# Optimization experiments

Hardware: AMD Instinct MI355X
Metric: run time of the kernel (lower is better)

## Reference

```python
import jax, jax.numpy as jnp
import numpy as np

N_SRC = 50000
N_DST = 10000
E = 1600000
H = 1
F = 128
NEG_SLOPE = 0.2  # GAT default leaky_relu slope


def setup_inputs() -> dict:
    key = jax.random.key(0)
    k1, k2, k3, k4, k5, k6 = jax.random.split(key, 6)
    x_src = jax.random.normal(k1, (N_SRC, H, F), dtype=jnp.float32)
    x_dst = jax.random.normal(k2, (N_DST, H, F), dtype=jnp.float32)
    attn_l = jax.random.normal(k3, (1, H, F), dtype=jnp.float32)
    attn_r = jax.random.normal(k4, (1, H, F), dtype=jnp.float32)
    src_idx = jax.random.randint(k5, (E,), 0, N_SRC, dtype=jnp.int64 if jax.config.jax_enable_x64 else jnp.int32)
    dst_idx = jnp.sort(jax.random.randint(k6, (E,), 0, N_DST, dtype=jnp.int64 if jax.config.jax_enable_x64 else jnp.int32))
    return {"x_src": x_src, "x_dst": x_dst, "attn_l": attn_l, "attn_r": attn_r,
            "src_idx": src_idx, "dst_idx": dst_idx}


def reference(x_src, x_dst, attn_l, attn_r, src_idx, dst_idx):
    n_dst = x_dst.shape[0]
    # per-node attention logits: [N, H]
    el = (x_src * attn_l).sum(axis=-1)
    er = (x_dst * attn_r).sum(axis=-1)
    # per-edge score e = leaky_relu(el[u] + er[v]): [E, H]
    e = jax.nn.leaky_relu(el[src_idx] + er[dst_idx], negative_slope=NEG_SLOPE)
    ex = jnp.exp(e)
    # segment-sum over destination neighborhoods: [N_dst, H]
    sum_ex = jax.ops.segment_sum(ex, dst_idx, num_segments=n_dst)
    attention = ex / sum_ex[dst_idx]  # [E, H]
    # attention-weighted gather of src features, scattered to dst: [N_dst, H, F]
    msg = attention[..., None] * x_src[src_idx]
    out = jax.ops.segment_sum(msg, dst_idx, num_segments=n_dst)
    return out
```

## Files before the change

kernel.cpp:

```cpp
#include <hip/hip_runtime.h>
#include <hip/hip_fp16.h>

#define F 128
#define NEG_SLOPE 0.2f

__global__ __launch_bounds__(256)
void prep_kernel(const float* __restrict__ x_src, const float* __restrict__ attn_l,
                 float* __restrict__ el, __half2* __restrict__ xh, int n_src,
                 const float* __restrict__ x_dst, const float* __restrict__ attn_r,
                 float* __restrict__ er, int n_dst,
                 const int* __restrict__ dst_idx, int* __restrict__ offs, int E,
                 int nlog) {
    if ((int)blockIdx.x < nlog) {
        int row  = blockIdx.x * 4 + (threadIdx.x >> 6);
        int lane = threadIdx.x & 63;
        if (row < n_src) {
            float2 xv = *reinterpret_cast<const float2*>(&x_src[(size_t)row * F + lane * 2]);
            float2 av = *reinterpret_cast<const float2*>(&attn_l[lane * 2]);
            if (xh) xh[(size_t)row * (F / 2) + lane] = __floats2half2_rn(xv.x, xv.y);
            float s = xv.x * av.x + xv.y * av.y;
            #pragma unroll
            for (int o = 32; o > 0; o >>= 1) s += __shfl_xor(s, o, 64);
            if (lane == 0) el[row] = s;
        } else if (row < n_src + n_dst) {
            int r = row - n_src;
            float2 xv = *reinterpret_cast<const float2*>(&x_dst[(size_t)r * F + lane * 2]);
            float2 av = *reinterpret_cast<const float2*>(&attn_r[lane * 2]);
            float s = xv.x * av.x + xv.y * av.y;
            #pragma unroll
            for (int o = 32; o > 0; o >>= 1) s += __shfl_xor(s, o, 64);
            if (lane == 0) er[r] = s;
        }
    } else {
        int e = ((int)blockIdx.x - nlog) * 256 + threadIdx.x;
        if (e >= E) return;
        int d = dst_idx[e];
        int prev = (e == 0) ? -1 : dst_idx[e - 1];
        for (int v = prev + 1; v <= d; ++v) offs[v] = e;
        if (e == E - 1)
            for (int v = d + 1; v <= n_dst; ++v) offs[v] = E;
    }
}

template<bool H>
__global__ __launch_bounds__(256)
void gat_aggregate_kernel(const __half2* __restrict__ xh,
                          const float* __restrict__ x_src,
                          const float* __restrict__ el,
                          const float* __restrict__ er,
                          const int* __restrict__ src_idx,
                          const int* __restrict__ offs,
                          float* __restrict__ out, int n_dst) {
    int v = blockIdx.x * 4 + (threadIdx.x >> 6);
    if (v >= n_dst) return;
    int lane = threadIdx.x & 63;
    int g    = lane >> 4;
    int l16  = lane & 15;

    int start = offs[v];
    int end   = offs[v + 1];
    int count = end - start;
    float erv = er[v];

    const float4* x4h = reinterpret_cast<const float4*>(xh);
    const float4* x4f = reinterpret_cast<const float4*>(x_src);

    float a0[8], a1[8];
    #pragma unroll
    for (int k = 0; k < 8; ++k) { a0[k] = 0.f; a1[k] = 0.f; }
    float d0 = 0.f, d1 = 0.f;

    int full = count & ~7;
    for (int it = 0; it < full; it += 8) {
        int e0 = start + it + g;
        int e1 = e0 + 4;
        int s0 = src_idx[e0];
        int s1 = src_idx[e1];
        float l0 = el[s0] + erv, l1 = el[s1] + erv;
        l0 = l0 > 0.f ? l0 : NEG_SLOPE * l0;
        l1 = l1 > 0.f ? l1 : NEG_SLOPE * l1;
        float w0 = __expf(l0), w1 = __expf(l1);
        d0 += w0; d1 += w1;
        if (H) {
            float4 r0 = x4h[(size_t)s0 * (F / 8) + l16];
            float4 r1 = x4h[(size_t)s1 * (F / 8) + l16];
            const __half2* h0 = reinterpret_cast<const __half2*>(&r0);
            const __half2* h1 = reinterpret_cast<const __half2*>(&r1);
            #pragma unroll
            for (int k = 0; k < 4; ++k) {
                float2 f0 = __half22float2(h0[k]);
                float2 f1 = __half22float2(h1[k]);
                a0[2*k]   += w0 * f0.x;  a0[2*k+1] += w0 * f0.y;
                a1[2*k]   += w1 * f1.x;  a1[2*k+1] += w1 * f1.y;
            }
        } else {
            float4 p0 = x4f[(size_t)s0 * (F / 4) + l16 * 2];
            float4 q0 = x4f[(size_t)s0 * (F / 4) + l16 * 2 + 1];
            float4 p1 = x4f[(size_t)s1 * (F / 4) + l16 * 2];
            float4 q1 = x4f[(size_t)s1 * (F / 4) + l16 * 2 + 1];
            a0[0]+=w0*p0.x; a0[1]+=w0*p0.y; a0[2]+=w0*p0.z; a0[3]+=w0*p0.w;
            a0[4]+=w0*q0.x; a0[5]+=w0*q0.y; a0[6]+=w0*q0.z; a0[7]+=w0*q0.w;
            a1[0]+=w1*p1.x; a1[1]+=w1*p1.y; a1[2]+=w1*p1.z; a1[3]+=w1*p1.w;
            a1[4]+=w1*q1.x; a1[5]+=w1*q1.y; a1[6]+=w1*q1.z; a1[7]+=w1*q1.w;
        }
    }
    for (int e = start + full + g; e < end; e += 4) {
        int s = src_idx[e];
        float l = el[s] + erv;
        l = l > 0.f ? l : NEG_SLOPE * l;
        float w = __expf(l);
        d0 += w;
        if (H) {
            float4 r = x4h[(size_t)s * (F / 8) + l16];
            const __half2* h = reinterpret_cast<const __half2*>(&r);
            #pragma unroll
            for (int k = 0; k < 4; ++k) {
                float2 f = __half22float2(h[k]);
                a0[2*k] += w * f.x;  a0[2*k+1] += w * f.y;
            }
        } else {
            float4 p = x4f[(size_t)s * (F / 4) + l16 * 2];
            float4 q = x4f[(size_t)s * (F / 4) + l16 * 2 + 1];
            a0[0]+=w*p.x; a0[1]+=w*p.y; a0[2]+=w*p.z; a0[3]+=w*p.w;
            a0[4]+=w*q.x; a0[5]+=w*q.y; a0[6]+=w*q.z; a0[7]+=w*q.w;
        }
    }
    #pragma unroll
    for (int k = 0; k < 8; ++k) a0[k] += a1[k];
    d0 += d1;

    #pragma unroll
    for (int k = 0; k < 8; ++k) {
        a0[k] += __shfl_xor(a0[k], 16, 64);
        a0[k] += __shfl_xor(a0[k], 32, 64);
    }
    d0 += __shfl_xor(d0, 16, 64);
    d0 += __shfl_xor(d0, 32, 64);

    if (g == 0) {
        float inv = (count > 0) ? 1.f / d0 : 0.f;
        float4 o0 = make_float4(a0[0]*inv, a0[1]*inv, a0[2]*inv, a0[3]*inv);
        float4 o1 = make_float4(a0[4]*inv, a0[5]*inv, a0[6]*inv, a0[7]*inv);
        float4* dst = reinterpret_cast<float4*>(&out[(size_t)v * F + l16 * 8]);
        dst[0] = o0;
        dst[1] = o1;
    }
}

extern "C" void kernel_launch(void* const* d_in, const int* in_sizes, int n_in,
                              void* d_out, int out_size, void* d_ws, size_t ws_size,
                              hipStream_t stream) {
    const float* x_src   = (const float*)d_in[0];
    const float* x_dst   = (const float*)d_in[1];
    const float* attn_l  = (const float*)d_in[2];
    const float* attn_r  = (const float*)d_in[3];
    const int*   src_idx = (const int*)d_in[4];
    const int*   dst_idx = (const int*)d_in[5];

    int n_src = in_sizes[0] / F;
    int n_dst = in_sizes[1] / F;
    int E     = in_sizes[4];

    float* out  = (float*)d_out;
    float* el   = (float*)d_ws;
    float* er   = el + n_src;
    int*   offs = (int*)(er + n_dst);
    uintptr_t p = (uintptr_t)(offs + n_dst + 1);
    p = (p + 15) & ~(uintptr_t)15;
    __half2* xh = (__half2*)p;

    size_t need = (p - (uintptr_t)d_ws) + (size_t)n_src * F * sizeof(__half);
    bool fp16ok = ws_size >= need;

    int nlog = (n_src + n_dst + 3) / 4;
    int noff = (E + 255) / 256;
    prep_kernel<<<nlog + noff, 256, 0, stream>>>(
        x_src, attn_l, el, fp16ok ? xh : nullptr, n_src,
        x_dst, attn_r, er, n_dst, dst_idx, offs, E, nlog);

    int agg_blocks = (n_dst + 3) / 4;
    if (fp16ok) {
        gat_aggregate_kernel<true><<<agg_blocks, 256, 0, stream>>>(
            xh, x_src, el, er, src_idx, offs, out, n_dst);
    } else {
        gat_aggregate_kernel<false><<<agg_blocks, 256, 0, stream>>>(
            nullptr, x_src, el, er, src_idx, offs, out, n_dst);
    }
}
```

Baseline: 86.93 us.

## Assign one block per destination and bucket edges by source range for locality

Each aggregation block now handles a single destination node with 256 threads instead of one wavefront per node. Edges are processed in chunks: weights are computed once into shared memory, then counting-sorted into 8 source-index buckets so that gathers within a chunk hit nearby rows. Partial sums across the four wavefronts are combined through shared memory. This adds several block barriers, shared atomics and more blocks per launch, in exchange for intended gather locality and higher per-node parallelism. With about 160 edges per node, all of them fit in one chunk.

```diff
diff --git a/kernel.cpp b/kernel.cpp
--- a/kernel.cpp
+++ b/kernel.cpp
@@ -3,6 +3,9 @@
 
 #define F 128
 #define NEG_SLOPE 0.2f
+#define NB 8
+#define CH 512
+#define NGR 16
 
 __global__ __launch_bounds__(256)
 void prep_kernel(const float* __restrict__ x_src, const float* __restrict__ attn_l,
@@ -50,18 +53,26 @@
                           const float* __restrict__ er,
                           const int* __restrict__ src_idx,
                           const int* __restrict__ offs,
-                          float* __restrict__ out, int n_dst) {
-    int v = blockIdx.x * 4 + (threadIdx.x >> 6);
-    if (v >= n_dst) return;
-    int lane = threadIdx.x & 63;
-    int g    = lane >> 4;
-    int l16  = lane & 15;
+                          float* __restrict__ out, int bdiv) {
+    int v   = blockIdx.x;
+    int tid = threadIdx.x;
+    int g   = tid >> 4;
+    int l16 = tid & 15;
 
     int start = offs[v];
     int end   = offs[v + 1];
     int count = end - start;
     float erv = er[v];
 
+    __shared__ int   sidx[CH];
+    __shared__ float sw[CH];
+    __shared__ int   bidx[CH];
+    __shared__ float bw[CH];
+    __shared__ int   cnt[NB];
+    __shared__ int   cur[NB];
+    __shared__ float part[4][F];
+    __shared__ float pden[4];
+
     const float4* x4h = reinterpret_cast<const float4*>(xh);
     const float4* x4f = reinterpret_cast<const float4*>(x_src);
 
@@ -70,61 +81,86 @@
     for (int k = 0; k < 8; ++k) { a0[k] = 0.f; a1[k] = 0.f; }
     float d0 = 0.f, d1 = 0.f;
 
-    int full = count & ~7;
-    for (int it = 0; it < full; it += 8) {
-        int e0 = start + it + g;
-        int e1 = e0 + 4;
-        int s0 = src_idx[e0];
-        int s1 = src_idx[e1];
-        float l0 = el[s0] + erv, l1 = el[s1] + erv;
-        l0 = l0 > 0.f ? l0 : NEG_SLOPE * l0;
-        l1 = l1 > 0.f ? l1 : NEG_SLOPE * l1;
-        float w0 = __expf(l0), w1 = __expf(l1);
-        d0 += w0; d1 += w1;
-        if (H) {
-            float4 r0 = x4h[(size_t)s0 * (F / 8) + l16];
-            float4 r1 = x4h[(size_t)s1 * (F / 8) + l16];
-            const __half2* h0 = reinterpret_cast<const __half2*>(&r0);
-            const __half2* h1 = reinterpret_cast<const __half2*>(&r1);
-            #pragma unroll
-            for (int k = 0; k < 4; ++k) {
-                float2 f0 = __half22float2(h0[k]);
-                float2 f1 = __half22float2(h1[k]);
-                a0[2*k]   += w0 * f0.x;  a0[2*k+1] += w0 * f0.y;
-                a1[2*k]   += w1 * f1.x;  a1[2*k+1] += w1 * f1.y;
+    for (int base = start; base < end; base += CH) {
+        int n = min(CH, end - base);
+        if (tid < NB) cnt[tid] = 0;
+        __syncthreads();
+
+        for (int i = tid; i < n; i += 256) {
+            int s = src_idx[base + i];
+            float l = el[s] + erv;
+            l = l > 0.f ? l : NEG_SLOPE * l;
+            sidx[i] = s;
+            sw[i]   = __expf(l);
+            atomicAdd(&cnt[s / bdiv], 1);
+        }
+        __syncthreads();
+        if (tid < NB) {
+            int acc = 0;
+            for (int b = 0; b < tid; ++b) acc += cnt[b];
+            cur[tid] = acc;
+        }
+        __syncthreads();
+        for (int i = tid; i < n; i += 256) {
+            int s = sidx[i];
+            int slot = atomicAdd(&cur[s / bdiv], 1);
+            bidx[slot] = s;
+            bw[slot]   = sw[i];
+        }
+        __syncthreads();
+
+        int full = n & ~(2 * NGR - 1);
+        for (int it = 0; it < full; it += 2 * NGR) {
+            int s0 = bidx[it + g];
+            int s1 = bidx[it + NGR + g];
+            float w0 = bw[it + g];
+            float w1 = bw[it + NGR + g];
+            d0 += w0; d1 += w1;
+            if (H) {
+                float4 r0 = x4h[(size_t)s0 * (F / 8) + l16];
+                float4 r1 = x4h[(size_t)s1 * (F / 8) + l16];
+                const __half2* h0 = reinterpret_cast<const __half2*>(&r0);
+                const __half2* h1 = reinterpret_cast<const __half2*>(&r1);
+                #pragma unroll
+                for (int k = 0; k < 4; ++k) {
+                    float2 f0 = __half22float2(h0[k]);
+                    float2 f1 = __half22float2(h1[k]);
+                    a0[2*k]   += w0 * f0.x;  a0[2*k+1] += w0 * f0.y;
+                    a1[2*k]   += w1 * f1.x;  a1[2*k+1] += w1 * f1.y;
+                }
+            } else {
+                float4 p0 = x4f[(size_t)s0 * (F/4) + l16*2];
+                float4 q0 = x4f[(size_t)s0 * (F/4) + l16*2 + 1];
+                float4 p1 = x4f[(size_t)s1 * (F/4) + l16*2];
+                float4 q1 = x4f[(size_t)s1 * (F/4) + l16*2 + 1];
+                a0[0]+=w0*p0.x; a0[1]+=w0*p0.y; a0[2]+=w0*p0.z; a0[3]+=w0*p0.w;
+                a0[4]+=w0*q0.x; a0[5]+=w0*q0.y; a0[6]+=w0*q0.z; a0[7]+=w0*q0.w;
+                a1[0]+=w1*p1.x; a1[1]+=w1*p1.y; a1[2]+=w1*p1.z; a1[3]+=w1*p1.w;
+                a1[4]+=w1*q1.x; a1[5]+=w1*q1.y; a1[6]+=w1*q1.z; a1[7]+=w1*q1.w;
             }
-        } else {
-            float4 p0 = x4f[(size_t)s0 * (F / 4) + l16 * 2];
-            float4 q0 = x4f[(size_t)s0 * (F / 4) + l16 * 2 + 1];
-            float4 p1 = x4f[(size_t)s1 * (F / 4) + l16 * 2];
-            float4 q1 = x4f[(size_t)s1 * (F / 4) + l16 * 2 + 1];
-            a0[0]+=w0*p0.x; a0[1]+=w0*p0.y; a0[2]+=w0*p0.z; a0[3]+=w0*p0.w;
-            a0[4]+=w0*q0.x; a0[5]+=w0*q0.y; a0[6]+=w0*q0.z; a0[7]+=w0*q0.w;
-            a1[0]+=w1*p1.x; a1[1]+=w1*p1.y; a1[2]+=w1*p1.z; a1[3]+=w1*p1.w;
-            a1[4]+=w1*q1.x; a1[5]+=w1*q1.y; a1[6]+=w1*q1.z; a1[7]+=w1*q1.w;
-        }
-    }
-    for (int e = start + full + g; e < end; e += 4) {
-        int s = src_idx[e];
-        float l = el[s] + erv;
-        l = l > 0.f ? l : NEG_SLOPE * l;
-        float w = __expf(l);
-        d0 += w;
-        if (H) {
-            float4 r = x4h[(size_t)s * (F / 8) + l16];
-            const __half2* h = reinterpret_cast<const __half2*>(&r);
-            #pragma unroll
-            for (int k = 0; k < 4; ++k) {
-                float2 f = __half22float2(h[k]);
-                a0[2*k] += w * f.x;  a0[2*k+1] += w * f.y;
+        }
+        for (int it = full + g; it < n; it += NGR) {
+            int s  = bidx[it];
+            float w = bw[it];
+            d0 += w;
+            if (H) {
+                float4 r = x4h[(size_t)s * (F / 8) + l16];
+                const __half2* h = reinterpret_cast<const __half2*>(&r);
+                #pragma unroll
+                for (int k = 0; k < 4; ++k) {
+                    float2 f = __half22float2(h[k]);
+                    a0[2*k] += w * f.x;  a0[2*k+1] += w * f.y;
+                }
+            } else {
+                float4 p = x4f[(size_t)s * (F/4) + l16*2];
+                float4 q = x4f[(size_t)s * (F/4) + l16*2 + 1];
+                a0[0]+=w*p.x; a0[1]+=w*p.y; a0[2]+=w*p.z; a0[3]+=w*p.w;
+                a0[4]+=w*q.x; a0[5]+=w*q.y; a0[6]+=w*q.z; a0[7]+=w*q.w;
             }
-        } else {
-            float4 p = x4f[(size_t)s * (F / 4) + l16 * 2];
-            float4 q = x4f[(size_t)s * (F / 4) + l16 * 2 + 1];
-            a0[0]+=w*p.x; a0[1]+=w*p.y; a0[2]+=w*p.z; a0[3]+=w*p.w;
-            a0[4]+=w*q.x; a0[5]+=w*q.y; a0[6]+=w*q.z; a0[7]+=w*q.w;
-        }
-    }
+        }
+        __syncthreads();
+    }
+
     #pragma unroll
     for (int k = 0; k < 8; ++k) a0[k] += a1[k];
     d0 += d1;
@@ -137,13 +173,20 @@
     d0 += __shfl_xor(d0, 16, 64);
     d0 += __shfl_xor(d0, 32, 64);
 
-    if (g == 0) {
-        float inv = (count > 0) ? 1.f / d0 : 0.f;
-        float4 o0 = make_float4(a0[0]*inv, a0[1]*inv, a0[2]*inv, a0[3]*inv);
-        float4 o1 = make_float4(a0[4]*inv, a0[5]*inv, a0[6]*inv, a0[7]*inv);
-        float4* dst = reinterpret_cast<float4*>(&out[(size_t)v * F + l16 * 8]);
-        dst[0] = o0;
-        dst[1] = o1;
+    int wid  = tid >> 6;
+    int lane = tid & 63;
+    if ((lane >> 4) == 0) {
+        #pragma unroll
+        for (int k = 0; k < 8; ++k) part[wid][l16 * 8 + k] = a0[k];
+        if (l16 == 0) pden[wid] = d0;
+    }
+    __syncthreads();
+
+    if (tid < F) {
+        float t = 0.f, dd = 0.f;
+        #pragma unroll
+        for (int w = 0; w < 4; ++w) { t += part[w][tid]; dd += pden[w]; }
+        out[(size_t)v * F + tid] = (count > 0) ? t / dd : 0.f;
     }
 }
 
@@ -178,12 +221,12 @@
         x_src, attn_l, el, fp16ok ? xh : nullptr, n_src,
         x_dst, attn_r, er, n_dst, dst_idx, offs, E, nlog);
 
-    int agg_blocks = (n_dst + 3) / 4;
+    int bdiv = (n_src + NB - 1) / NB;
     if (fp16ok) {
-        gat_aggregate_kernel<true><<<agg_blocks, 256, 0, stream>>>(
-            xh, x_src, el, er, src_idx, offs, out, n_dst);
+        gat_aggregate_kernel<true><<<n_dst, 256, 0, stream>>>(
+            xh, x_src, el, er, src_idx, offs, out, bdiv);
     } else {
-        gat_aggregate_kernel<false><<<agg_blocks, 256, 0, stream>>>(
-            nullptr, x_src, el, er, src_idx, offs, out, n_dst);
+        gat_aggregate_kernel<false><<<n_dst, 256, 0, stream>>>(
+            nullptr, x_src, el, er, src_idx, offs, out, bdiv);
     }
 }
```

Result: faster. 80.09 us (-7.9%).

## Partition edges by source-node range and aggregate in cache-sized passes

Applied to the files above, without the earlier changes.

Adds a reorder kernel that buckets each destination's edges into four source-index ranges, then runs the aggregation in four passes, one per range. Each pass only gathers from about a quarter of the fp16 feature table, so that slice should stay resident in the L2 or last-level cache. In exchange it adds a reorder kernel with many block syncs, extra launches, and re-reads and re-writes of the output and a denominator buffer between passes.

```diff
diff --git a/kernel.cpp b/kernel.cpp
--- a/kernel.cpp
+++ b/kernel.cpp
@@ -3,6 +3,7 @@
 
 #define F 128
 #define NEG_SLOPE 0.2f
+#define NB 4
 
 __global__ __launch_bounds__(256)
 void prep_kernel(const float* __restrict__ x_src, const float* __restrict__ attn_l,
@@ -42,24 +43,72 @@
     }
 }
 
+__global__ __launch_bounds__(256)
+void reorder_kernel(const int* __restrict__ src_idx, const int* __restrict__ offs,
+                    int* __restrict__ src_r, int* __restrict__ boffs,
+                    int n_dst, int bdiv) {
+    int v   = blockIdx.x;
+    int tid = threadIdx.x;
+    int start = offs[v], end = offs[v + 1];
+
+    __shared__ int cnt[NB];
+    __shared__ int base_[NB];
+    __shared__ int wtot[4];
+
+    if (tid < NB) cnt[tid] = 0;
+    __syncthreads();
+    for (int i = start + tid; i < end; i += 256)
+        atomicAdd(&cnt[src_idx[i] / bdiv], 1);
+    __syncthreads();
+    if (tid == 0) {
+        int acc = start;
+        #pragma unroll
+        for (int b = 0; b < NB; ++b) {
+            base_[b] = acc;
+            boffs[(size_t)v * (NB + 1) + b] = acc;
+            acc += cnt[b];
+        }
+        boffs[(size_t)v * (NB + 1) + NB] = acc;
+    }
+    __syncthreads();
+
+    int lane = tid & 63, wid = tid >> 6;
+    for (int cbase = start; cbase < end; cbase += 256) {
+        int n = end - cbase; if (n > 256) n = 256;
+        int s = 0, b = -1;
+        if (tid < n) { s = src_idx[cbase + tid]; b = s / bdiv; }
+        #pragma unroll
+        for (int bb = 0; bb < NB; ++bb) {
+            bool flag = (b == bb);
+            unsigned long long m = __ballot(flag);
+            int rk = __popcll(m & ((1ULL << lane) - 1ULL));
+            if (lane == 0) wtot[wid] = __popcll(m);
+            __syncthreads();
+            int wpre = 0;
+            for (int w = 0; w < wid; ++w) wpre += wtot[w];
+            if (flag) src_r[base_[bb] + wpre + rk] = s;
+            __syncthreads();
+            if (tid == 0) base_[bb] += wtot[0] + wtot[1] + wtot[2] + wtot[3];
+            __syncthreads();
+        }
+    }
+}
+
 template<bool H>
 __global__ __launch_bounds__(256)
-void gat_aggregate_kernel(const __half2* __restrict__ xh,
-                          const float* __restrict__ x_src,
-                          const float* __restrict__ el,
-                          const float* __restrict__ er,
-                          const int* __restrict__ src_idx,
-                          const int* __restrict__ offs,
-                          float* __restrict__ out, int n_dst) {
+void agg_kernel(const __half2* __restrict__ xh, const float* __restrict__ x_src,
+                const float* __restrict__ el, const float* __restrict__ er,
+                const int* __restrict__ src_r, const int* __restrict__ boffs,
+                int nbp1, int b, float* __restrict__ out, float* __restrict__ den_ws,
+                int n_dst, int first, int last) {
     int v = blockIdx.x * 4 + (threadIdx.x >> 6);
     if (v >= n_dst) return;
     int lane = threadIdx.x & 63;
     int g    = lane >> 4;
     int l16  = lane & 15;
 
-    int start = offs[v];
-    int end   = offs[v + 1];
-    int count = end - start;
+    int s0e = boffs[(size_t)v * nbp1 + b];
+    int s1e = boffs[(size_t)v * nbp1 + b + 1];
     float erv = er[v];
 
     const float4* x4h = reinterpret_cast<const float4*>(xh);
@@ -70,12 +119,13 @@
     for (int k = 0; k < 8; ++k) { a0[k] = 0.f; a1[k] = 0.f; }
     float d0 = 0.f, d1 = 0.f;
 
-    int full = count & ~7;
+    int count = s1e - s0e;
+    int full  = count & ~7;
     for (int it = 0; it < full; it += 8) {
-        int e0 = start + it + g;
+        int e0 = s0e + it + g;
         int e1 = e0 + 4;
-        int s0 = src_idx[e0];
-        int s1 = src_idx[e1];
+        int s0 = src_r[e0];
+        int s1 = src_r[e1];
         float l0 = el[s0] + erv, l1 = el[s1] + erv;
         l0 = l0 > 0.f ? l0 : NEG_SLOPE * l0;
         l1 = l1 > 0.f ? l1 : NEG_SLOPE * l1;
@@ -94,18 +144,18 @@
                 a1[2*k]   += w1 * f1.x;  a1[2*k+1] += w1 * f1.y;
             }
         } else {
-            float4 p0 = x4f[(size_t)s0 * (F / 4) + l16 * 2];
-            float4 q0 = x4f[(size_t)s0 * (F / 4) + l16 * 2 + 1];
-            float4 p1 = x4f[(size_t)s1 * (F / 4) + l16 * 2];
-            float4 q1 = x4f[(size_t)s1 * (F / 4) + l16 * 2 + 1];
+            float4 p0 = x4f[(size_t)s0 * (F/4) + l16*2];
+            float4 q0 = x4f[(size_t)s0 * (F/4) + l16*2 + 1];
+            float4 p1 = x4f[(size_t)s1 * (F/4) + l16*2];
+            float4 q1 = x4f[(size_t)s1 * (F/4) + l16*2 + 1];
             a0[0]+=w0*p0.x; a0[1]+=w0*p0.y; a0[2]+=w0*p0.z; a0[3]+=w0*p0.w;
             a0[4]+=w0*q0.x; a0[5]+=w0*q0.y; a0[6]+=w0*q0.z; a0[7]+=w0*q0.w;
             a1[0]+=w1*p1.x; a1[1]+=w1*p1.y; a1[2]+=w1*p1.z; a1[3]+=w1*p1.w;
             a1[4]+=w1*q1.x; a1[5]+=w1*q1.y; a1[6]+=w1*q1.z; a1[7]+=w1*q1.w;
         }
     }
-    for (int e = start + full + g; e < end; e += 4) {
-        int s = src_idx[e];
+    for (int e = s0e + full + g; e < s1e; e += 4) {
+        int s = src_r[e];
         float l = el[s] + erv;
         l = l > 0.f ? l : NEG_SLOPE * l;
         float w = __expf(l);
@@ -119,8 +169,8 @@
                 a0[2*k] += w * f.x;  a0[2*k+1] += w * f.y;
             }
         } else {
-            float4 p = x4f[(size_t)s * (F / 4) + l16 * 2];
-            float4 q = x4f[(size_t)s * (F / 4) + l16 * 2 + 1];
+            float4 p = x4f[(size_t)s * (F/4) + l16*2];
+            float4 q = x4f[(size_t)s * (F/4) + l16*2 + 1];
             a0[0]+=w*p.x; a0[1]+=w*p.y; a0[2]+=w*p.z; a0[3]+=w*p.w;
             a0[4]+=w*q.x; a0[5]+=w*q.y; a0[6]+=w*q.z; a0[7]+=w*q.w;
         }
@@ -138,12 +188,28 @@
     d0 += __shfl_xor(d0, 32, 64);
 
     if (g == 0) {
-        float inv = (count > 0) ? 1.f / d0 : 0.f;
-        float4 o0 = make_float4(a0[0]*inv, a0[1]*inv, a0[2]*inv, a0[3]*inv);
-        float4 o1 = make_float4(a0[4]*inv, a0[5]*inv, a0[6]*inv, a0[7]*inv);
-        float4* dst = reinterpret_cast<float4*>(&out[(size_t)v * F + l16 * 8]);
-        dst[0] = o0;
-        dst[1] = o1;
+        float4* po = reinterpret_cast<float4*>(&out[(size_t)v * F + l16 * 8]);
+        float4 o0, o1;
+        float dprev = 0.f;
+        if (first) {
+            o0 = make_float4(0.f, 0.f, 0.f, 0.f);
+            o1 = o0;
+        } else {
+            o0 = po[0]; o1 = po[1];
+            dprev = den_ws[v];
+        }
+        o0.x += a0[0]; o0.y += a0[1]; o0.z += a0[2]; o0.w += a0[3];
+        o1.x += a0[4]; o1.y += a0[5]; o1.z += a0[6]; o1.w += a0[7];
+        float dtot = dprev + d0;
+        if (last) {
+            float inv = (dtot > 0.f) ? 1.f / dtot : 0.f;
+            o0.x *= inv; o0.y *= inv; o0.z *= inv; o0.w *= inv;
+            o1.x *= inv; o1.y *= inv; o1.z *= inv; o1.w *= inv;
+        } else if (l16 == 0) {
+            den_ws[v] = dtot;
+        }
+        po[0] = o0;
+        po[1] = o1;
     }
 }
 
@@ -168,9 +234,15 @@
     uintptr_t p = (uintptr_t)(offs + n_dst + 1);
     p = (p + 15) & ~(uintptr_t)15;
     __half2* xh = (__half2*)p;
-
-    size_t need = (p - (uintptr_t)d_ws) + (size_t)n_src * F * sizeof(__half);
-    bool fp16ok = ws_size >= need;
+    uintptr_t q = p + (size_t)n_src * F * sizeof(__half);
+    int*   src_r  = (int*)q;
+    int*   boffs  = src_r + E;
+    float* den_ws = (float*)(boffs + (size_t)n_dst * (NB + 1));
+
+    size_t need_fp16 = (p - (uintptr_t)d_ws) + (size_t)n_src * F * sizeof(__half);
+    size_t need_full = ((uintptr_t)(den_ws + n_dst)) - (uintptr_t)d_ws;
+    bool fp16ok = ws_size >= need_fp16;
+    bool fullok = ws_size >= need_full;
 
     int nlog = (n_src + n_dst + 3) / 4;
     int noff = (E + 255) / 256;
@@ -179,11 +251,20 @@
         x_dst, attn_r, er, n_dst, dst_idx, offs, E, nlog);
 
     int agg_blocks = (n_dst + 3) / 4;
-    if (fp16ok) {
-        gat_aggregate_kernel<true><<<agg_blocks, 256, 0, stream>>>(
-            xh, x_src, el, er, src_idx, offs, out, n_dst);
+    if (fullok && fp16ok) {
+        int bdiv = (n_src + NB - 1) / NB;
+        reorder_kernel<<<n_dst, 256, 0, stream>>>(src_idx, offs, src_r, boffs,
+                                                  n_dst, bdiv);
+        for (int b = 0; b < NB; ++b) {
+            agg_kernel<true><<<agg_blocks, 256, 0, stream>>>(
+                xh, nullptr, el, er, src_r, boffs, NB + 1, b, out, den_ws,
+                n_dst, b == 0 ? 1 : 0, b == NB - 1 ? 1 : 0);
+        }
+    } else if (fp16ok) {
+        agg_kernel<true><<<agg_blocks, 256, 0, stream>>>(
+            xh, nullptr, el, er, src_idx, offs, 1, 0, out, nullptr, n_dst, 1, 1);
     } else {
-        gat_aggregate_kernel<false><<<agg_blocks, 256, 0, stream>>>(
-            nullptr, x_src, el, er, src_idx, offs, out, n_dst);
-    }
-}
+        agg_kernel<false><<<agg_blocks, 256, 0, stream>>>(
+            nullptr, x_src, el, er, src_idx, offs, 1, 0, out, nullptr, n_dst, 1, 1);
+    }
+}
```

Measured after the change: 98.60 us. 1.13x slower.

## Split fp16 features into column slabs and precompute per-edge weights

Applied to the files above, without the earlier changes.

The fp16 copy of x_src is stored as four feature-column slabs of 32 halves each, so every aggregation block handles one slab and its gather footprint is smaller and friendlier to cache. Edge weights are computed once per edge in a new kernel, which removes the repeated el gather and exp from the aggregation loop. Accumulation uses v_fma_mix to multiply-add fp16 inputs into fp32 directly, and prep now processes two rows per wave with float4 loads. The cost is an extra kernel launch, an E-sized weight buffer, four times as many index loads across slices, and a larger workspace requirement; if the workspace is too small, the code falls back to fp32.

```diff
diff --git a/kernel.cpp b/kernel.cpp
--- a/kernel.cpp
+++ b/kernel.cpp
@@ -3,34 +3,48 @@
 
 #define F 128
 #define NEG_SLOPE 0.2f
+#define NB 4
+
+#define FMA_MIX_LO(acc, w, h) \
+    asm("v_fma_mix_f32 %0, %1, %2, %0 op_sel:[0,0,0] op_sel_hi:[0,1,0]" \
+        : "+v"(acc) : "v"(w), "v"(h))
+#define FMA_MIX_HI(acc, w, h) \
+    asm("v_fma_mix_f32 %0, %1, %2, %0 op_sel:[0,1,0] op_sel_hi:[0,1,0]" \
+        : "+v"(acc) : "v"(w), "v"(h))
 
 __global__ __launch_bounds__(256)
 void prep_kernel(const float* __restrict__ x_src, const float* __restrict__ attn_l,
-                 float* __restrict__ el, __half2* __restrict__ xh, int n_src,
+                 float* __restrict__ el, __half* __restrict__ xh, int n_src,
                  const float* __restrict__ x_dst, const float* __restrict__ attn_r,
                  float* __restrict__ er, int n_dst,
                  const int* __restrict__ dst_idx, int* __restrict__ offs, int E,
                  int nlog) {
     if ((int)blockIdx.x < nlog) {
-        int row  = blockIdx.x * 4 + (threadIdx.x >> 6);
+        int wave = blockIdx.x * 4 + (threadIdx.x >> 6);
         int lane = threadIdx.x & 63;
-        if (row < n_src) {
-            float2 xv = *reinterpret_cast<const float2*>(&x_src[(size_t)row * F + lane * 2]);
-            float2 av = *reinterpret_cast<const float2*>(&attn_l[lane * 2]);
-            if (xh) xh[(size_t)row * (F / 2) + lane] = __floats2half2_rn(xv.x, xv.y);
-            float s = xv.x * av.x + xv.y * av.y;
-            #pragma unroll
-            for (int o = 32; o > 0; o >>= 1) s += __shfl_xor(s, o, 64);
-            if (lane == 0) el[row] = s;
-        } else if (row < n_src + n_dst) {
-            int r = row - n_src;
-            float2 xv = *reinterpret_cast<const float2*>(&x_dst[(size_t)r * F + lane * 2]);
-            float2 av = *reinterpret_cast<const float2*>(&attn_r[lane * 2]);
-            float s = xv.x * av.x + xv.y * av.y;
-            #pragma unroll
-            for (int o = 32; o > 0; o >>= 1) s += __shfl_xor(s, o, 64);
-            if (lane == 0) er[r] = s;
+        int half = lane >> 5;
+        int l32  = lane & 31;
+        int row  = wave * 2 + half;
+        const float* x; const float* attn; float* o; int r; bool is_src;
+        if (row < n_src)              { x = x_src; attn = attn_l; o = el; r = row; is_src = true; }
+        else if (row < n_src + n_dst) { x = x_dst; attn = attn_r; o = er; r = row - n_src; is_src = false; }
+        else return;
+        float4 xv = reinterpret_cast<const float4*>(x)[(size_t)r * 32 + l32];
+        float4 av = reinterpret_cast<const float4*>(attn)[l32];
+        if (xh && is_src) {
+            __half2 h0 = __floats2half2_rn(xv.x, xv.y);
+            __half2 h1 = __floats2half2_rn(xv.z, xv.w);
+            uint2 u;
+            u.x = *reinterpret_cast<unsigned int*>(&h0);
+            u.y = *reinterpret_cast<unsigned int*>(&h1);
+            int bsl = l32 >> 3;
+            int ch  = l32 & 7;
+            reinterpret_cast<uint2*>(xh)[(size_t)bsl * n_src * 8 + (size_t)r * 8 + ch] = u;
         }
+        float s = xv.x * av.x + xv.y * av.y + xv.z * av.z + xv.w * av.w;
+        #pragma unroll
+        for (int o_ = 16; o_ > 0; o_ >>= 1) s += __shfl_xor(s, o_, 64);
+        if (l32 == 0) o[r] = s;
     } else {
         int e = ((int)blockIdx.x - nlog) * 256 + threadIdx.x;
         if (e >= E) return;
@@ -42,15 +56,97 @@
     }
 }
 
-template<bool H>
-__global__ __launch_bounds__(256)
-void gat_aggregate_kernel(const __half2* __restrict__ xh,
-                          const float* __restrict__ x_src,
-                          const float* __restrict__ el,
-                          const float* __restrict__ er,
-                          const int* __restrict__ src_idx,
-                          const int* __restrict__ offs,
-                          float* __restrict__ out, int n_dst) {
+__global__ __launch_bounds__(256)
+void weight_kernel(const float* __restrict__ el, const float* __restrict__ er,
+                   const int* __restrict__ src_idx, const int* __restrict__ dst_idx,
+                   float* __restrict__ w, int E) {
+    int e = blockIdx.x * 256 + threadIdx.x;
+    if (e >= E) return;
+    float l = el[src_idx[e]] + er[dst_idx[e]];
+    l = l > 0.f ? l : NEG_SLOPE * l;
+    w[e] = __expf(l);
+}
+
+__global__ __launch_bounds__(256)
+void agg_fslice_kernel(const __half* __restrict__ xh,
+                       const float* __restrict__ wbuf,
+                       const int* __restrict__ src_idx,
+                       const int* __restrict__ offs,
+                       float* __restrict__ out, int n_dst, int n_src) {
+    int b = blockIdx.x & (NB - 1);
+    int v = ((int)blockIdx.x >> 2) * 4 + (threadIdx.x >> 6);
+    if (v >= n_dst) return;
+    int lane = threadIdx.x & 63;
+    int slot = lane >> 2;
+    int fq   = lane & 3;
+
+    int s0e = offs[v];
+    int s1e = offs[v + 1];
+    int cnt = s1e - s0e;
+
+    const uint4* slab = reinterpret_cast<const uint4*>(xh) + (size_t)b * n_src * 4;
+
+    float a[8];
+    #pragma unroll
+    for (int k = 0; k < 8; ++k) a[k] = 0.f;
+    float den = 0.f;
+
+    int full = cnt & ~31;
+    for (int it = 0; it < full; it += 32) {
+        int e0 = s0e + it + slot;
+        int e1 = e0 + 16;
+        int s0 = src_idx[e0];
+        int s1 = src_idx[e1];
+        float w0 = wbuf[e0];
+        float w1 = wbuf[e1];
+        uint4 r0 = slab[(size_t)s0 * 4 + fq];
+        uint4 r1 = slab[(size_t)s1 * 4 + fq];
+        den += w0 + w1;
+        FMA_MIX_LO(a[0], w0, r0.x);  FMA_MIX_HI(a[1], w0, r0.x);
+        FMA_MIX_LO(a[2], w0, r0.y);  FMA_MIX_HI(a[3], w0, r0.y);
+        FMA_MIX_LO(a[4], w0, r0.z);  FMA_MIX_HI(a[5], w0, r0.z);
+        FMA_MIX_LO(a[6], w0, r0.w);  FMA_MIX_HI(a[7], w0, r0.w);
+        FMA_MIX_LO(a[0], w1, r1.x);  FMA_MIX_HI(a[1], w1, r1.x);
+        FMA_MIX_LO(a[2], w1, r1.y);  FMA_MIX_HI(a[3], w1, r1.y);
+        FMA_MIX_LO(a[4], w1, r1.z);  FMA_MIX_HI(a[5], w1, r1.z);
+        FMA_MIX_LO(a[6], w1, r1.w);  FMA_MIX_HI(a[7], w1, r1.w);
+    }
+    for (int e = s0e + full + slot; e < s1e; e += 16) {
+        int s = src_idx[e];
+        float w = wbuf[e];
+        uint4 r = slab[(size_t)s * 4 + fq];
+        den += w;
+        FMA_MIX_LO(a[0], w, r.x);  FMA_MIX_HI(a[1], w, r.x);
+        FMA_MIX_LO(a[2], w, r.y);  FMA_MIX_HI(a[3], w, r.y);
+        FMA_MIX_LO(a[4], w, r.z);  FMA_MIX_HI(a[5], w, r.z);
+        FMA_MIX_LO(a[6], w, r.w);  FMA_MIX_HI(a[7], w, r.w);
+    }
+
+    #pragma unroll
+    for (int k = 0; k < 8; ++k) {
+        a[k] += __shfl_xor(a[k], 4, 64);
+        a[k] += __shfl_xor(a[k], 8, 64);
+        a[k] += __shfl_xor(a[k], 16, 64);
+        a[k] += __shfl_xor(a[k], 32, 64);
+    }
+    den += __shfl_xor(den, 4, 64);
+    den += __shfl_xor(den, 8, 64);
+    den += __shfl_xor(den, 16, 64);
+    den += __shfl_xor(den, 32, 64);
+
+    if (slot == 0) {
+        float inv = (cnt > 0) ? 1.f / den : 0.f;
+        float4* dst = reinterpret_cast<float4*>(&out[(size_t)v * F + b * 32 + fq * 8]);
+        dst[0] = make_float4(a[0]*inv, a[1]*inv, a[2]*inv, a[3]*inv);
+        dst[1] = make_float4(a[4]*inv, a[5]*inv, a[6]*inv, a[7]*inv);
+    }
+}
+
+__global__ __launch_bounds__(256)
+void agg_full_kernel(const float* __restrict__ x_src,
+                     const float* __restrict__ el, const float* __restrict__ er,
+                     const int* __restrict__ src_idx, const int* __restrict__ offs,
+                     float* __restrict__ out, int n_dst) {
     int v = blockIdx.x * 4 + (threadIdx.x >> 6);
     if (v >= n_dst) return;
     int lane = threadIdx.x & 63;
@@ -62,73 +158,24 @@
     int count = end - start;
     float erv = er[v];
 
-    const float4* x4h = reinterpret_cast<const float4*>(xh);
     const float4* x4f = reinterpret_cast<const float4*>(x_src);
 
-    float a0[8], a1[8];
-    #pragma unroll
-    for (int k = 0; k < 8; ++k) { a0[k] = 0.f; a1[k] = 0.f; }
-    float d0 = 0.f, d1 = 0.f;
-
-    int full = count & ~7;
-    for (int it = 0; it < full; it += 8) {
-        int e0 = start + it + g;
-        int e1 = e0 + 4;
-        int s0 = src_idx[e0];
-        int s1 = src_idx[e1];
-        float l0 = el[s0] + erv, l1 = el[s1] + erv;
-        l0 = l0 > 0.f ? l0 : NEG_SLOPE * l0;
-        l1 = l1 > 0.f ? l1 : NEG_SLOPE * l1;
-        float w0 = __expf(l0), w1 = __expf(l1);
-        d0 += w0; d1 += w1;
-        if (H) {
-            float4 r0 = x4h[(size_t)s0 * (F / 8) + l16];
-            float4 r1 = x4h[(size_t)s1 * (F / 8) + l16];
-            const __half2* h0 = reinterpret_cast<const __half2*>(&r0);
-            const __half2* h1 = reinterpret_cast<const __half2*>(&r1);
-            #pragma unroll
-            for (int k = 0; k < 4; ++k) {
-                float2 f0 = __half22float2(h0[k]);
-                float2 f1 = __half22float2(h1[k]);
-                a0[2*k]   += w0 * f0.x;  a0[2*k+1] += w0 * f0.y;
-                a1[2*k]   += w1 * f1.x;  a1[2*k+1] += w1 * f1.y;
-            }
-        } else {
-            float4 p0 = x4f[(size_t)s0 * (F / 4) + l16 * 2];
-            float4 q0 = x4f[(size_t)s0 * (F / 4) + l16 * 2 + 1];
-            float4 p1 = x4f[(size_t)s1 * (F / 4) + l16 * 2];
-            float4 q1 = x4f[(size_t)s1 * (F / 4) + l16 * 2 + 1];
-            a0[0]+=w0*p0.x; a0[1]+=w0*p0.y; a0[2]+=w0*p0.z; a0[3]+=w0*p0.w;
-            a0[4]+=w0*q0.x; a0[5]+=w0*q0.y; a0[6]+=w0*q0.z; a0[7]+=w0*q0.w;
-            a1[0]+=w1*p1.x; a1[1]+=w1*p1.y; a1[2]+=w1*p1.z; a1[3]+=w1*p1.w;
-            a1[4]+=w1*q1.x; a1[5]+=w1*q1.y; a1[6]+=w1*q1.z; a1[7]+=w1*q1.w;
-        }
-    }
-    for (int e = start + full + g; e < end; e += 4) {
+    float a0[8];
+    #pragma unroll
+    for (int k = 0; k < 8; ++k) a0[k] = 0.f;
+    float d0 = 0.f;
+
+    for (int e = start + g; e < end; e += 4) {
         int s = src_idx[e];
         float l = el[s] + erv;
         l = l > 0.f ? l : NEG_SLOPE * l;
         float w = __expf(l);
         d0 += w;
-        if (H) {
-            float4 r = x4h[(size_t)s * (F / 8) + l16];
-            const __half2* h = reinterpret_cast<const __half2*>(&r);
-            #pragma unroll
-            for (int k = 0; k < 4; ++k) {
-                float2 f = __half22float2(h[k]);
-                a0[2*k] += w * f.x;  a0[2*k+1] += w * f.y;
-            }
-        } else {
-            float4 p = x4f[(size_t)s * (F / 4) + l16 * 2];
-            float4 q = x4f[(size_t)s * (F / 4) + l16 * 2 + 1];
-            a0[0]+=w*p.x; a0[1]+=w*p.y; a0[2]+=w*p.z; a0[3]+=w*p.w;
-            a0[4]+=w*q.x; a0[5]+=w*q.y; a0[6]+=w*q.z; a0[7]+=w*q.w;
-        }
-    }
-    #pragma unroll
-    for (int k = 0; k < 8; ++k) a0[k] += a1[k];
-    d0 += d1;
-
+        float4 p = x4f[(size_t)s * (F/4) + l16*2];
+        float4 q = x4f[(size_t)s * (F/4) + l16*2 + 1];
+        a0[0]+=w*p.x; a0[1]+=w*p.y; a0[2]+=w*p.z; a0[3]+=w*p.w;
+        a0[4]+=w*q.x; a0[5]+=w*q.y; a0[6]+=w*q.z; a0[7]+=w*q.w;
+    }
     #pragma unroll
     for (int k = 0; k < 8; ++k) {
         a0[k] += __shfl_xor(a0[k], 16, 64);
@@ -139,11 +186,9 @@
 
     if (g == 0) {
         float inv = (count > 0) ? 1.f / d0 : 0.f;
-        float4 o0 = make_float4(a0[0]*inv, a0[1]*inv, a0[2]*inv, a0[3]*inv);
-        float4 o1 = make_float4(a0[4]*inv, a0[5]*inv, a0[6]*inv, a0[7]*inv);
         float4* dst = reinterpret_cast<float4*>(&out[(size_t)v * F + l16 * 8]);
-        dst[0] = o0;
-        dst[1] = o1;
+        dst[0] = make_float4(a0[0]*inv, a0[1]*inv, a0[2]*inv, a0[3]*inv);
+        dst[1] = make_float4(a0[4]*inv, a0[5]*inv, a0[6]*inv, a0[7]*inv);
     }
 }
 
@@ -167,23 +212,31 @@
     int*   offs = (int*)(er + n_dst);
     uintptr_t p = (uintptr_t)(offs + n_dst + 1);
     p = (p + 15) & ~(uintptr_t)15;
-    __half2* xh = (__half2*)p;
-
-    size_t need = (p - (uintptr_t)d_ws) + (size_t)n_src * F * sizeof(__half);
-    bool fp16ok = ws_size >= need;
-
-    int nlog = (n_src + n_dst + 3) / 4;
+    __half* xh  = (__half*)p;
+    uintptr_t q = p + (size_t)n_src * F * sizeof(__half);
+    q = (q + 15) & ~(uintptr_t)15;
+    float* w    = (float*)q;
+
+    size_t need_full = (q - (uintptr_t)d_ws) + (size_t)E * sizeof(float);
+    bool fullok = ws_size >= need_full;
+
+    int nlog = (n_src + n_dst + 7) / 8;
     int noff = (E + 255) / 256;
-    prep_kernel<<<nlog + noff, 256, 0, stream>>>(
-        x_src, attn_l, el, fp16ok ? xh : nullptr, n_src,
-        x_dst, attn_r, er, n_dst, dst_idx, offs, E, nlog);
-
-    int agg_blocks = (n_dst + 3) / 4;
-    if (fp16ok) {
-        gat_aggregate_kernel<true><<<agg_blocks, 256, 0, stream>>>(
-            xh, x_src, el, er, src_idx, offs, out, n_dst);
+
+    if (fullok) {
+        prep_kernel<<<nlog + noff, 256, 0, stream>>>(
+            x_src, attn_l, el, xh, n_src,
+            x_dst, attn_r, er, n_dst, dst_idx, offs, E, nlog);
+        weight_kernel<<<(E + 255) / 256, 256, 0, stream>>>(
+            el, er, src_idx, dst_idx, w, E);
+        int ngrp = (n_dst + 3) / 4;
+        agg_fslice_kernel<<<ngrp * NB, 256, 0, stream>>>(
+            xh, w, src_idx, offs, out, n_dst, n_src);
     } else {
-        gat_aggregate_kernel<false><<<agg_blocks, 256, 0, stream>>>(
-            nullptr, x_src, el, er, src_idx, offs, out, n_dst);
-    }
-}
+        prep_kernel<<<nlog + noff, 256, 0, stream>>>(
+            x_src, attn_l, el, nullptr, n_src,
+            x_dst, attn_r, er, n_dst, dst_idx, offs, E, nlog);
+        agg_full_kernel<<<(n_dst + 3) / 4, 256, 0, stream>>>(
+            x_src, el, er, src_idx, offs, out, n_dst);
+    }
+}
```

After: 77.88 us. -10.4%, faster.
